# Optimization experiments

Hardware: AMD Instinct MI355X
Metric: run time of the kernel (lower is better)

## Reference

```python
import jax, jax.numpy as jnp
import numpy as np

NUM_VERTS = 6890
NUM_JOINTS = 24
NUM_BETAS = 10
NUM_POSE_BASIS = 207  # 23 joints * 9 rotmat entries
BATCH = 1024
# SMPL kinematic tree; root's parent set to 0 (root handled separately in FK loop)
PARENTS = np.array([0, 0, 0, 0, 1, 2, 3, 4, 5, 6, 7, 8, 9, 9, 9, 12, 13, 14, 16, 17, 18, 19, 20, 21], dtype=np.int32)


def rodrigues(rot_vecs):
    """Axis-angle [..., 3] -> rotation matrices [..., 3, 3] (batch_rodrigues)."""
    angle = jnp.linalg.norm(rot_vecs + 1e-8, axis=-1, keepdims=True)  # [...,1]
    rot_dir = rot_vecs / angle
    cos = jnp.cos(angle)[..., None]
    sin = jnp.sin(angle)[..., None]
    rx, ry, rz = rot_dir[..., 0], rot_dir[..., 1], rot_dir[..., 2]
    zeros = jnp.zeros_like(rx)
    K = jnp.stack([zeros, -rz, ry, rz, zeros, -rx, -ry, rx, zeros], axis=-1)
    K = K.reshape(rot_vecs.shape[:-1] + (3, 3))
    outer = rot_dir[..., :, None] * rot_dir[..., None, :]
    eye = jnp.eye(3, dtype=rot_vecs.dtype)
    return cos * eye + (1.0 - cos) * outer + sin * K


def setup_inputs() -> dict:
    key = jax.random.key(0)
    ks = jax.random.split(key, 9)
    pose_axis_angle = 0.2 * jax.random.normal(ks[0], (BATCH, 69), dtype=jnp.float32)
    betas = jax.random.normal(ks[1], (BATCH, NUM_BETAS), dtype=jnp.float32)
    global_orient = 0.2 * jax.random.normal(ks[2], (BATCH, 3), dtype=jnp.float32)
    v_template = jax.random.normal(ks[3], (NUM_VERTS, 3), dtype=jnp.float32) * 0.3
    shapedirs = jax.random.normal(ks[4], (NUM_VERTS, 3, NUM_BETAS), dtype=jnp.float32) * 0.01
    posedirs = jax.random.normal(ks[5], (NUM_POSE_BASIS, NUM_VERTS * 3), dtype=jnp.float32) * 0.001
    jr = jax.random.uniform(ks[6], (NUM_JOINTS, NUM_VERTS), dtype=jnp.float32)
    J_regressor = jr / jnp.sum(jr, axis=1, keepdims=True)
    jr17 = jax.random.uniform(ks[7], (17, NUM_VERTS), dtype=jnp.float32)
    J_regressor_h36m = jr17 / jnp.sum(jr17, axis=1, keepdims=True)
    w = jax.random.uniform(ks[8], (NUM_VERTS, NUM_JOINTS), dtype=jnp.float32)
    lbs_weights = w / jnp.sum(w, axis=1, keepdims=True)
    return {
        'pose_axis_angle': pose_axis_angle, 'betas': betas, 'global_orient': global_orient,
        'v_template': v_template, 'shapedirs': shapedirs, 'posedirs': posedirs,
        'J_regressor': J_regressor, 'J_regressor_h36m': J_regressor_h36m,
        'lbs_weights': lbs_weights,
    }


def lbs(betas, full_pose, v_template, shapedirs, posedirs, J_regressor, J_regressor_h36m, lbs_weights):
    B = betas.shape[0]
    dt = betas.dtype
    # 1) shape blendshapes
    v_shaped = v_template[None] + jnp.einsum('bl,vcl->bvc', betas, shapedirs)  # [B,V,3]
    # 2) rest-pose joints
    J = jnp.einsum('jv,bvc->bjc', J_regressor, v_shaped)  # [B,24,3]
    # 3) per-joint rotation matrices from axis-angle
    rot_mats = rodrigues(full_pose.reshape(B, NUM_JOINTS, 3))  # [B,24,3,3]
    # 4) pose blendshapes (rotations minus identity, excluding root)
    pose_feature = (rot_mats[:, 1:] - jnp.eye(3, dtype=dt)).reshape(B, NUM_POSE_BASIS)
    v_posed = v_shaped + (pose_feature @ posedirs).reshape(B, NUM_VERTS, 3)
    # 5) forward kinematics along the tree
    rel_joints = J.at[:, 1:].add(-J[:, PARENTS[1:]])  # [B,24,3]
    T_local = jnp.concatenate([
        jnp.concatenate([rot_mats, rel_joints[..., None]], axis=-1),           # [B,24,3,4]
        jnp.broadcast_to(jnp.array([0., 0., 0., 1.], dtype=dt), (B, NUM_JOINTS, 1, 4)),
    ], axis=-2)  # [B,24,4,4]
    chain = [T_local[:, 0]]
    for i in range(1, NUM_JOINTS):
        chain.append(chain[PARENTS[i]] @ T_local[:, i])
    transforms = jnp.stack(chain, axis=1)  # [B,24,4,4] global transforms
    posed_joints = transforms[:, :, :3, 3]  # [B,24,3]
    # relative transforms: subtract R_global @ J_rest from translation column
    rel_trans = transforms[:, :, :3, 3] - jnp.einsum('bjmn,bjn->bjm', transforms[:, :, :3, :3], J)
    A = transforms.at[:, :, :3, 3].set(rel_trans)  # [B,24,4,4]
    # 6) skinning
    T = jnp.einsum('vj,bjmn->bvmn', lbs_weights, A)  # [B,V,4,4]
    verts = jnp.einsum('bvmn,bvn->bvm', T[:, :, :3, :3], v_posed) + T[:, :, :3, 3]  # [B,V,3]
    joints_from_verts = jnp.einsum('jv,bvc->bjc', J_regressor_h36m, verts)  # [B,17,3]
    return verts, posed_joints, rot_mats, joints_from_verts


def reference(pose_axis_angle, betas, global_orient, v_template, shapedirs, posedirs, J_regressor, J_regressor_h36m, lbs_weights):
    full_pose = jnp.concatenate([global_orient, pose_axis_angle], axis=1)  # [B,72]
    verts, joints, rot_mats, j17 = lbs(betas, full_pose, v_template, shapedirs, posedirs,
                                       J_regressor, J_regressor_h36m, lbs_weights)
    # transl is None branch: root-center (root offsets are detached in torch)
    root17 = jax.lax.stop_gradient(j17[:, 0:1])
    vertices = verts - root17
    joints = joints - jax.lax.stop_gradient(joints[:, 0:1])
    joints_from_verts = j17 - root17
    return vertices, joints, joints_from_verts, rot_mats
```

## Files before the change

kernel.cpp:

```cpp
#include <hip/hip_runtime.h>
#include <math.h>

#define B 1024
#define NV 6890
#define NP 207
#define KP 224
#define NR 20736
#define VTB 256
#define BT 16

typedef float fx2 __attribute__((ext_vector_type(2)));
typedef float fx4 __attribute__((ext_vector_type(4)));
typedef short s8v __attribute__((ext_vector_type(8)));
typedef float f4v __attribute__((ext_vector_type(4)));

#define OFF_J   21166080
#define OFF_J17 21239808
#define OFF_R   21292032

#define WSB_A    0
#define WSB_JRX  1179648
#define WSB_PF32 1183744
#define WSB_PFB  2035712
#define WSB_PDT  2494464

__device__ __constant__ int PAR[24] = {0,0,0,0,1,2,3,4,5,6,7,8,9,9,9,12,13,14,16,17,18,19,20,21};

__device__ inline unsigned short f2bf(float f) {
  unsigned int u = __builtin_bit_cast(unsigned int, f);
  unsigned int r = (u + 0x7FFFu + ((u >> 16) & 1u)) >> 16;
  return (unsigned short)r;
}

__global__ __launch_bounds__(256) void k_jrx(const float* __restrict__ JR,
    const float* __restrict__ vtm, const float* __restrict__ sd,
    float* __restrict__ JRX) {
  int o = blockIdx.x;
  int j = o / 3, c = o % 3;
  float acc[11];
#pragma unroll
  for (int q = 0; q < 11; q++) acc[q] = 0.f;
  for (int v = threadIdx.x; v < NV; v += 256) {
    float r = JR[(size_t)j * NV + v];
    acc[0] += r * vtm[(size_t)v * 3 + c];
    const float* s = sd + (size_t)v * 30 + c * 10;
#pragma unroll
    for (int l = 0; l < 10; l++) acc[1 + l] += r * s[l];
  }
#pragma unroll
  for (int q = 0; q < 11; q++) {
    for (int off = 32; off; off >>= 1) acc[q] += __shfl_xor(acc[q], off, 64);
  }
  __shared__ float red[4][11];
  int wave = threadIdx.x >> 6, lane = threadIdx.x & 63;
  if (lane == 0) {
#pragma unroll
    for (int q = 0; q < 11; q++) red[wave][q] = acc[q];
  }
  __syncthreads();
  if (threadIdx.x < 11) {
    int q = threadIdx.x;
    JRX[o * 11 + q] = red[0][q] + red[1][q] + red[2][q] + red[3][q];
  }
}

__global__ __launch_bounds__(128) void k_pose(const float* __restrict__ go,
    const float* __restrict__ paa, const float* __restrict__ betas,
    const float* __restrict__ JRX, float* __restrict__ rot_out,
    float* __restrict__ joints_out, float* __restrict__ pf32,
    unsigned short* __restrict__ pfb, float* __restrict__ A, int write_pfb) {
  int b = blockIdx.x, t = threadIdx.x;
  __shared__ float Rl[24][9];
  __shared__ float Jl[24][3];
  __shared__ float Cl[24][12];
  __shared__ float pfl[KP];

  for (int i = t; i < KP; i += 128) pfl[i] = 0.f;
  __syncthreads();

  if (t < 24) {
    float x, y, z;
    if (t == 0) { x = go[b*3]; y = go[b*3+1]; z = go[b*3+2]; }
    else { const float* p = paa + (size_t)b*69 + (t-1)*3; x = p[0]; y = p[1]; z = p[2]; }
    float xe = x + 1e-8f, ye = y + 1e-8f, ze = z + 1e-8f;
    float ang = sqrtf(xe*xe + ye*ye + ze*ze);
    float inv = 1.f / ang;
    float rx = x*inv, ry = y*inv, rz = z*inv;
    float cc = cosf(ang), ss = sinf(ang), mc = 1.f - cc;
    float R[9];
    R[0]=cc+mc*rx*rx;    R[1]=mc*rx*ry-ss*rz; R[2]=mc*rx*rz+ss*ry;
    R[3]=mc*ry*rx+ss*rz; R[4]=cc+mc*ry*ry;    R[5]=mc*ry*rz-ss*rx;
    R[6]=mc*rz*rx-ss*ry; R[7]=mc*rz*ry+ss*rx; R[8]=cc+mc*rz*rz;
#pragma unroll
    for (int q = 0; q < 9; q++) {
      Rl[t][q] = R[q];
      rot_out[(size_t)b*216 + t*9 + q] = R[q];
    }
    if (t > 0) {
#pragma unroll
      for (int q = 0; q < 9; q++) {
        float pv = R[q] - ((q==0||q==4||q==8) ? 1.f : 0.f);
        pfl[(t-1)*9 + q] = pv;
        pf32[(size_t)b*208 + (t-1)*9 + q] = pv;
      }
    }
  }
  if (t < 10) pfl[NP + t] = betas[(size_t)b*10 + t];
  if (t < 72) {
    int j = t / 3;
    const float* x = JRX + t * 11;
    float s = x[0];
#pragma unroll
    for (int l = 0; l < 10; l++) s += betas[(size_t)b*10 + l] * x[1 + l];
    Jl[j][t % 3] = s;
  }
  __syncthreads();
  if (t < 12) {
    int m = t >> 2, n = t & 3;
    Cl[0][t] = (n < 3) ? Rl[0][m*3+n] : Jl[0][m];
  }
  __syncthreads();
  for (int i = 1; i < 24; i++) {
    int p = PAR[i];
    if (t < 12) {
      int m = t >> 2, n = t & 3;
      float v;
      if (n < 3)
        v = Cl[p][m*4+0]*Rl[i][0*3+n] + Cl[p][m*4+1]*Rl[i][1*3+n] + Cl[p][m*4+2]*Rl[i][2*3+n];
      else {
        float r0 = Jl[i][0]-Jl[p][0], r1 = Jl[i][1]-Jl[p][1], r2 = Jl[i][2]-Jl[p][2];
        v = Cl[p][m*4+0]*r0 + Cl[p][m*4+1]*r1 + Cl[p][m*4+2]*r2 + Cl[p][m*4+3];
      }
      Cl[i][t] = v;
    }
    __syncthreads();
  }
  if (t < 72) {
    int j = t / 3, c = t % 3;
    joints_out[(size_t)b*72 + t] = Cl[j][c*4+3] - Cl[0][c*4+3];
  }
  for (int idx = t; idx < 288; idx += 128) {
    int j = idx / 12, r = idx % 12, m = r >> 2, n = r & 3;
    float v;
    if (n < 3) v = Cl[j][m*4+n];
    else v = Cl[j][m*4+3] - (Cl[j][m*4+0]*Jl[j][0] + Cl[j][m*4+1]*Jl[j][1] + Cl[j][m*4+2]*Jl[j][2]);
    A[(size_t)b*288 + idx] = v;
  }
  if (write_pfb && t < 112) {
    unsigned int val = (unsigned int)f2bf(pfl[2*t]) |
                       ((unsigned int)f2bf(pfl[2*t+1]) << 16);
    ((unsigned int*)(pfb + (size_t)b * KP))[t] = val;
  }
}

#define VTC 64
__global__ __launch_bounds__(256) void k_cvt(const float* __restrict__ pd,
    const float* __restrict__ sd, unsigned short* __restrict__ pdt, int C0) {
  __shared__ unsigned short tt[VTC][KP + 8];
  int l0 = blockIdx.x * VTC;
  int n0 = C0 + l0;
  for (int i = threadIdx.x; i < VTC * (KP + 8) / 2; i += 256)
    ((unsigned int*)tt)[i] = 0u;
  __syncthreads();
  for (int idx = threadIdx.x; idx < NP * VTC; idx += 256) {
    int k = idx >> 6, n = idx & 63;
    int g = n0 + n;
    float v = (g < NV * 3) ? pd[(size_t)k * (NV * 3) + g] : 0.f;
    tt[n][k] = f2bf(v);
  }
  for (int idx = threadIdx.x; idx < 10 * VTC; idx += 256) {
    int n = idx / 10, l = idx % 10;
    int g = n0 + n;
    float v = 0.f;
    if (g < NV * 3) { int vv = g / 3, c = g % 3; v = sd[(size_t)vv * 30 + c * 10 + l]; }
    tt[n][NP + l] = f2bf(v);
  }
  __syncthreads();
  for (int i = threadIdx.x; i < VTC * (KP / 2); i += 256) {
    int row = i / (KP / 2), col = i % (KP / 2);
    unsigned int val = ((unsigned int)tt[row][2 * col]) |
                       (((unsigned int)tt[row][2 * col + 1]) << 16);
    ((unsigned int*)pdt)[(size_t)(l0 + row) * (KP / 2) + col] = val;
  }
}

#define VPLD 772
__global__ __launch_bounds__(256) void k_fused(
    const unsigned short* __restrict__ pfb,
    const unsigned short* __restrict__ pdt,
    const float* __restrict__ A,
    const float* __restrict__ w,
    const float* __restrict__ vtm,
    float* __restrict__ verts, int C0) {
  int b0 = blockIdx.x * BT;
  int lr0 = blockIdx.y * (VTB * 3);
  int v0 = C0 / 3 + blockIdx.y * VTB;
  int t = threadIdx.x;
  int lane = t & 63;
  int wv = t >> 6;

  __shared__ unsigned int pfA[16 * 116];
  __shared__ float vp[16 * VPLD];

  {
    const unsigned int* src = (const unsigned int*)(pfb + (size_t)b0 * KP);
#pragma unroll
    for (int i = 0; i < 7; i++) {
      int d = t + i * 256;
      pfA[(d / 112) * 116 + (d % 112)] = src[d];
    }
  }
  __syncthreads();

  int q = lane >> 4;
  int m = lane & 15;
  s8v af[7];
  {
    const unsigned int* arow = pfA + m * 116 + q * 4;
#pragma unroll
    for (int ks = 0; ks < 7; ks++) af[ks] = *(const s8v*)(arow + ks * 16);
  }
  const unsigned short* browb = pdt + (size_t)(lr0 + wv * 192 + m) * KP + q * 8;
#pragma unroll 1
  for (int f = 0; f < 12; f++) {
    const unsigned short* br = browb + (size_t)f * 16 * KP;
    f4v acc = {0.f, 0.f, 0.f, 0.f};
#pragma unroll
    for (int ks = 0; ks < 7; ks++)
      acc = __builtin_amdgcn_mfma_f32_16x16x32_bf16(af[ks], *(const s8v*)(br + ks * 32), acc, 0, 0, 0);
    int cbase = wv * 192 + f * 16 + m;
#pragma unroll
    for (int r = 0; r < 4; r++) vp[(q * 4 + r) * VPLD + cbase] = acc[r];
  }
  __syncthreads();

  int vglob = v0 + t;
  bool valid = vglob < NV;
  int vc = valid ? vglob : NV - 1;
  float wr[24];
  {
    const fx4* w4 = (const fx4*)(w + (size_t)vc * 24);
#pragma unroll
    for (int k = 0; k < 6; k++) {
      fx4 t4 = w4[k];
      wr[4*k]=t4.x; wr[4*k+1]=t4.y; wr[4*k+2]=t4.z; wr[4*k+3]=t4.w;
    }
  }
  float vt0 = vtm[(size_t)vc*3+0], vt1 = vtm[(size_t)vc*3+1], vt2 = vtm[(size_t)vc*3+2];

#pragma unroll 1
  for (int ib = 0; ib < BT; ib++) {
    const float* Ab = A + (size_t)(b0 + ib) * 288;
    float T[12];
#pragma unroll
    for (int r = 0; r < 12; r++) T[r] = 0.f;
#pragma unroll
    for (int j = 0; j < 24; j++) {
      float wj = wr[j];
      const fx4* a4 = (const fx4*)(Ab + j * 12);
      fx4 qa = a4[0], qb = a4[1], qc = a4[2];
      T[0]+=wj*qa.x; T[1]+=wj*qa.y; T[2]+=wj*qa.z;  T[3]+=wj*qa.w;
      T[4]+=wj*qb.x; T[5]+=wj*qb.y; T[6]+=wj*qb.z;  T[7]+=wj*qb.w;
      T[8]+=wj*qc.x; T[9]+=wj*qc.y; T[10]+=wj*qc.z; T[11]+=wj*qc.w;
    }
    float px = vp[ib * VPLD + t*3+0] + vt0;
    float py = vp[ib * VPLD + t*3+1] + vt1;
    float pz = vp[ib * VPLD + t*3+2] + vt2;
    float o0 = T[0]*px + T[1]*py + T[2]*pz  + T[3];
    float o1 = T[4]*px + T[5]*py + T[6]*pz  + T[7];
    float o2 = T[8]*px + T[9]*py + T[10]*pz + T[11];
    if (valid) {
      float* dst = verts + ((size_t)(b0 + ib) * NV + vglob) * 3;
      dst[0] = o0; dst[1] = o1; dst[2] = o2;
    }
  }
}

__global__ __launch_bounds__(256) void k_verts(
    const float* __restrict__ betas, const float* __restrict__ vt,
    const float* __restrict__ sd, const float* __restrict__ pd,
    const float* __restrict__ w, const float* __restrict__ pf,
    const float* __restrict__ A, float* __restrict__ verts) {
  int vbase = blockIdx.y * 256;
  int vraw = vbase + threadIdx.x;
  bool valid = vraw < NV;
  int v = valid ? vraw : (NV - 1);
  int b0 = blockIdx.x * BT;

  float sdr[30];
  {
    const fx2* s2 = (const fx2*)(sd + (size_t)v * 30);
#pragma unroll
    for (int q = 0; q < 15; q++) { fx2 tv = s2[q]; sdr[2*q] = tv.x; sdr[2*q+1] = tv.y; }
  }
  float vt0 = vt[(size_t)v*3+0], vt1 = vt[(size_t)v*3+1], vt2 = vt[(size_t)v*3+2];

  float acc[BT][3];
#pragma unroll
  for (int i = 0; i < BT; i++) {
    const float* be = betas + (size_t)(b0 + i) * 10;
    float a0 = vt0, a1 = vt1, a2 = vt2;
#pragma unroll
    for (int l = 0; l < 10; l++) {
      float bl = be[l];
      a0 += bl * sdr[l]; a1 += bl * sdr[10+l]; a2 += bl * sdr[20+l];
    }
    acc[i][0] = a0; acc[i][1] = a1; acc[i][2] = a2;
  }

  const float* pcol = pd + 3 * (size_t)v;
  float cur[12], nxt[12];
#pragma unroll
  for (int r = 0; r < 4; r++) {
    const float* rp = pcol + (size_t)r * 20670;
    cur[3*r] = rp[0]; cur[3*r+1] = rp[1]; cur[3*r+2] = rp[2];
  }
#pragma unroll 1
  for (int k = 0; k < 204; k += 4) {
    if (k < 200) {
#pragma unroll
      for (int r = 0; r < 4; r++) {
        const float* rp = pcol + (size_t)(k + 4 + r) * 20670;
        nxt[3*r] = rp[0]; nxt[3*r+1] = rp[1]; nxt[3*r+2] = rp[2];
      }
    }
#pragma unroll
    for (int i = 0; i < BT; i++) {
      fx4 q = *(const fx4*)(pf + (size_t)(b0 + i) * 208 + k);
      acc[i][0] += q.x*cur[0] + q.y*cur[3] + q.z*cur[6] + q.w*cur[9];
      acc[i][1] += q.x*cur[1] + q.y*cur[4] + q.z*cur[7] + q.w*cur[10];
      acc[i][2] += q.x*cur[2] + q.y*cur[5] + q.z*cur[8] + q.w*cur[11];
    }
#pragma unroll
    for (int r = 0; r < 12; r++) cur[r] = nxt[r];
  }
  {
    float p00,p01,p02,p10,p11,p12,p20,p21,p22;
    { const float* r = pcol + (size_t)204*20670; p00=r[0]; p01=r[1]; p02=r[2]; }
    { const float* r = pcol + (size_t)205*20670; p10=r[0]; p11=r[1]; p12=r[2]; }
    { const float* r = pcol + (size_t)206*20670; p20=r[0]; p21=r[1]; p22=r[2]; }
#pragma unroll
    for (int i = 0; i < BT; i++) {
      const float* pb = pf + (size_t)(b0 + i) * 208;
      float q0 = pb[204], q1 = pb[205], q2 = pb[206];
      acc[i][0] += q0*p00 + q1*p10 + q2*p20;
      acc[i][1] += q0*p01 + q1*p11 + q2*p21;
      acc[i][2] += q0*p02 + q1*p12 + q2*p22;
    }
  }

  float wr[24];
  {
    const fx4* w4 = (const fx4*)(w + (size_t)v * 24);
#pragma unroll
    for (int q = 0; q < 6; q++) {
      fx4 t4 = w4[q];
      wr[4*q]=t4.x; wr[4*q+1]=t4.y; wr[4*q+2]=t4.z; wr[4*q+3]=t4.w;
    }
  }

#pragma unroll 1
  for (int i = 0; i < BT; i++) {
    const float* Ab = A + (size_t)(b0 + i) * 288;
    float T[12];
#pragma unroll
    for (int q = 0; q < 12; q++) T[q] = 0.f;
#pragma unroll
    for (int j = 0; j < 24; j++) {
      float wj = wr[j];
      const fx4* a4 = (const fx4*)(Ab + j * 12);
      fx4 qa = a4[0], qb = a4[1], qc = a4[2];
      T[0]+=wj*qa.x; T[1]+=wj*qa.y; T[2]+=wj*qa.z;  T[3]+=wj*qa.w;
      T[4]+=wj*qb.x; T[5]+=wj*qb.y; T[6]+=wj*qb.z;  T[7]+=wj*qb.w;
      T[8]+=wj*qc.x; T[9]+=wj*qc.y; T[10]+=wj*qc.z; T[11]+=wj*qc.w;
    }
    float x = acc[i][0], y = acc[i][1], z = acc[i][2];
    float o0 = T[0]*x + T[1]*y + T[2]*z  + T[3];
    float o1 = T[4]*x + T[5]*y + T[6]*z  + T[7];
    float o2 = T[8]*x + T[9]*y + T[10]*z + T[11];
    if (valid) {
      float* dst = verts + ((size_t)(b0 + i) * NV + vraw) * 3;
      dst[0] = o0; dst[1] = o1; dst[2] = o2;
    }
  }
}

__global__ __launch_bounds__(256) void k_j17s(const float* __restrict__ jrh,
    float* __restrict__ verts, float* __restrict__ j17_out) {
  int b = blockIdx.x;
  float acc[17][3];
#pragma unroll
  for (int j = 0; j < 17; j++) { acc[j][0]=0.f; acc[j][1]=0.f; acc[j][2]=0.f; }
  float* vb = verts + (size_t)b * NV * 3;
  for (int v = threadIdx.x; v < NV; v += 256) {
    float x = vb[v*3], y = vb[v*3+1], z = vb[v*3+2];
#pragma unroll
    for (int j = 0; j < 17; j++) {
      float r = jrh[(size_t)j * NV + v];
      acc[j][0] += r*x; acc[j][1] += r*y; acc[j][2] += r*z;
    }
  }
#pragma unroll
  for (int j = 0; j < 17; j++) {
#pragma unroll
    for (int c = 0; c < 3; c++) {
      for (int off = 32; off; off >>= 1) acc[j][c] += __shfl_xor(acc[j][c], off, 64);
    }
  }
  __shared__ float red[4][51];
  __shared__ float fin[51];
  int wave = threadIdx.x >> 6, lane = threadIdx.x & 63;
  if (lane == 0) {
#pragma unroll
    for (int j = 0; j < 17; j++) {
      red[wave][j*3+0] = acc[j][0]; red[wave][j*3+1] = acc[j][1]; red[wave][j*3+2] = acc[j][2];
    }
  }
  __syncthreads();
  if (threadIdx.x < 51)
    fin[threadIdx.x] = red[0][threadIdx.x] + red[1][threadIdx.x] + red[2][threadIdx.x] + red[3][threadIdx.x];
  __syncthreads();
  if (threadIdx.x < 51) {
    int c = threadIdx.x % 3;
    j17_out[(size_t)b*51 + threadIdx.x] = fin[threadIdx.x] - fin[c];
  }
  float r0 = fin[0], r1 = fin[1], r2 = fin[2];
  for (int idx = threadIdx.x; idx < NV * 3; idx += 256) {
    int c = idx % 3;
    float rr = (c == 0) ? r0 : (c == 1 ? r1 : r2);
    vb[idx] -= rr;
  }
}

extern "C" void kernel_launch(void* const* d_in, const int* in_sizes, int n_in,
                              void* d_out, int out_size, void* d_ws, size_t ws_size,
                              hipStream_t stream) {
  const float* pose  = (const float*)d_in[0];
  const float* betas = (const float*)d_in[1];
  const float* glob  = (const float*)d_in[2];
  const float* vtm   = (const float*)d_in[3];
  const float* sd    = (const float*)d_in[4];
  const float* pd    = (const float*)d_in[5];
  const float* JR    = (const float*)d_in[6];
  const float* JRh   = (const float*)d_in[7];
  const float* w     = (const float*)d_in[8];
  float* out = (float*)d_out;
  char* wsb = (char*)d_ws;
  float* A             = (float*)(wsb + WSB_A);
  float* JRX           = (float*)(wsb + WSB_JRX);
  float* pf32          = (float*)(wsb + WSB_PF32);
  unsigned short* pfb  = (unsigned short*)(wsb + WSB_PFB);
  unsigned short* pdt  = (unsigned short*)(wsb + WSB_PDT);

  int nch;
  if      (ws_size >= (size_t)2494464 + (size_t)NR * 448)        nch = 1;
  else if (ws_size >= (size_t)2494464 + (size_t)(NR/3) * 448)    nch = 3;
  else                                                           nch = 0;

  k_jrx<<<72, 256, 0, stream>>>(JR, vtm, sd, JRX);
  k_pose<<<B, 128, 0, stream>>>(glob, pose, betas, JRX, out + OFF_R, out + OFF_J,
                                pf32, pfb, A, nch ? 1 : 0);
  if (nch) {
    int CH = NR / nch;
    for (int c = 0; c < nch; c++) {
      k_cvt<<<CH / VTC, 256, 0, stream>>>(pd, sd, pdt, c * CH);
      k_fused<<<dim3(B / BT, CH / (VTB * 3)), 256, 0, stream>>>(pfb, pdt, A, w, vtm,
                                                                out, c * CH);
    }
  } else {
    k_verts<<<dim3(B / BT, 27), 256, 0, stream>>>(betas, vtm, sd, pd, w, pf32, A, out);
  }
  k_j17s<<<B, 256, 0, stream>>>(JRh, out, out + OFF_J17);
}
```

Baseline: 413.1 us.

## Store posed offsets as bf16 in aliased LDS, raise occupancy, vectorize root subtraction

```diff
diff --git a/kernel.cpp b/kernel.cpp
--- a/kernel.cpp
+++ b/kernel.cpp
@@ -8,6 +8,7 @@
 #define NR 20736
 #define VTB 256
 #define BT 16
+#define VPS 20
 
 typedef float fx2 __attribute__((ext_vector_type(2)));
 typedef float fx4 __attribute__((ext_vector_type(4)));
@@ -184,8 +185,7 @@
   }
 }
 
-#define VPLD 772
-__global__ __launch_bounds__(256) void k_fused(
+__global__ __launch_bounds__(256, 5) void k_fused(
     const unsigned short* __restrict__ pfb,
     const unsigned short* __restrict__ pdt,
     const float* __restrict__ A,
@@ -199,8 +199,9 @@
   int lane = t & 63;
   int wv = t >> 6;
 
-  __shared__ unsigned int pfA[16 * 116];
-  __shared__ float vp[16 * VPLD];
+  __shared__ unsigned long long smraw[768 * VPS / 4];
+  unsigned int* pfA = (unsigned int*)smraw;
+  unsigned short* vpb = (unsigned short*)smraw;
 
   {
     const unsigned int* src = (const unsigned int*)(pfb + (size_t)b0 * KP);
@@ -220,6 +221,8 @@
 #pragma unroll
     for (int ks = 0; ks < 7; ks++) af[ks] = *(const s8v*)(arow + ks * 16);
   }
+  __syncthreads();
+
   const unsigned short* browb = pdt + (size_t)(lr0 + wv * 192 + m) * KP + q * 8;
 #pragma unroll 1
   for (int f = 0; f < 12; f++) {
@@ -228,9 +231,11 @@
 #pragma unroll
     for (int ks = 0; ks < 7; ks++)
       acc = __builtin_amdgcn_mfma_f32_16x16x32_bf16(af[ks], *(const s8v*)(br + ks * 32), acc, 0, 0, 0);
-    int cbase = wv * 192 + f * 16 + m;
-#pragma unroll
-    for (int r = 0; r < 4; r++) vp[(q * 4 + r) * VPLD + cbase] = acc[r];
+    int comp = wv * 192 + f * 16 + m;
+    unsigned int lo = (unsigned int)f2bf(acc[0]) | ((unsigned int)f2bf(acc[1]) << 16);
+    unsigned int hi = (unsigned int)f2bf(acc[2]) | ((unsigned int)f2bf(acc[3]) << 16);
+    *(unsigned long long*)(vpb + comp * VPS + q * 4) =
+        (unsigned long long)lo | ((unsigned long long)hi << 32);
   }
   __syncthreads();
 
@@ -263,9 +268,12 @@
       T[4]+=wj*qb.x; T[5]+=wj*qb.y; T[6]+=wj*qb.z;  T[7]+=wj*qb.w;
       T[8]+=wj*qc.x; T[9]+=wj*qc.y; T[10]+=wj*qc.z; T[11]+=wj*qc.w;
     }
-    float px = vp[ib * VPLD + t*3+0] + vt0;
-    float py = vp[ib * VPLD + t*3+1] + vt1;
-    float pz = vp[ib * VPLD + t*3+2] + vt2;
+    unsigned int u0 = vpb[(t*3+0) * VPS + ib];
+    unsigned int u1 = vpb[(t*3+1) * VPS + ib];
+    unsigned int u2 = vpb[(t*3+2) * VPS + ib];
+    float px = __builtin_bit_cast(float, u0 << 16) + vt0;
+    float py = __builtin_bit_cast(float, u1 << 16) + vt1;
+    float pz = __builtin_bit_cast(float, u2 << 16) + vt2;
     float o0 = T[0]*px + T[1]*py + T[2]*pz  + T[3];
     float o1 = T[4]*px + T[5]*py + T[6]*pz  + T[7];
     float o2 = T[8]*px + T[9]*py + T[10]*pz + T[11];
@@ -425,10 +433,16 @@
     j17_out[(size_t)b*51 + threadIdx.x] = fin[threadIdx.x] - fin[c];
   }
   float r0 = fin[0], r1 = fin[1], r2 = fin[2];
-  for (int idx = threadIdx.x; idx < NV * 3; idx += 256) {
-    int c = idx % 3;
-    float rr = (c == 0) ? r0 : (c == 1 ? r1 : r2);
-    vb[idx] -= rr;
+  fx2* vb2 = (fx2*)vb;
+  for (int idx = threadIdx.x; idx < 10335; idx += 256) {
+    int f0 = idx * 2;
+    int c0 = f0 % 3;
+    int c1 = c0 + 1; if (c1 == 3) c1 = 0;
+    float s0 = (c0 == 0) ? r0 : ((c0 == 1) ? r1 : r2);
+    float s1 = (c1 == 0) ? r0 : ((c1 == 1) ? r1 : r2);
+    fx2 x = vb2[idx];
+    x.x -= s0; x.y -= s1;
+    vb2[idx] = x;
   }
 }
 
```

After: 346.8 us. -16.0%, faster.
